# Kernel optimization log

Hardware: AMD Instinct MI355X
Metric: run time of the kernel (lower is better)

Reference implementation:

```python
import jax, jax.numpy as jnp
import numpy as np

N_NODES = 50000
NEG_SLOPE = 0.2

def _leaky(x):
    return jnp.where(x > 0, x, NEG_SLOPE * x)

def _magic_conv(h, src, dst, edge_attr, anet_W, anet_b, mlp_W, mlp_b, eps):
    # align edge features to node dim: [E, d_in]
    e = edge_attr @ anet_W + anet_b
    # message: relu(x_j + edge), gather from source nodes
    msg = jax.nn.relu(h[src] + e)
    # scatter-add aggregate to target nodes: [N, d_in]
    agg = jax.ops.segment_sum(msg, dst, num_segments=N_NODES)
    # GIN-style update: cat([agg, (1+eps)*x]) -> Linear -> LeakyReLU(0.2)
    z = jnp.concatenate([agg, (1.0 + eps) * h], axis=-1) @ mlp_W + mlp_b
    return _leaky(z)

def setup_inputs() -> dict:
    key = jax.random.key(0)
    ks = jax.random.split(key, 16)
    E, D, DE = 800000, 128, 64
    inp = {
        "x": jax.random.normal(ks[0], (N_NODES, D), dtype=jnp.float32),
        "edge_index": jax.random.randint(ks[1], (2, E), 0, N_NODES, dtype=jnp.int64),
        "edge_attr": jax.random.normal(ks[2], (E, DE), dtype=jnp.float32),
    }
    s = lambda d: 1.0 / np.sqrt(d)
    # conv layer 0 (128 -> 128) and layer 1 (128 -> 128)
    for l, k0 in [(0, 3), (1, 8)]:
        inp[f"anet_W{l}"] = jax.random.uniform(ks[k0], (DE, D), jnp.float32, -s(DE), s(DE))
        inp[f"anet_b{l}"] = jax.random.uniform(ks[k0 + 1], (D,), jnp.float32, -s(DE), s(DE))
        inp[f"mlp_W{l}"] = jax.random.uniform(ks[k0 + 2], (2 * D, D), jnp.float32, -s(2 * D), s(2 * D))
        inp[f"mlp_b{l}"] = jax.random.uniform(ks[k0 + 3], (D,), jnp.float32, -s(2 * D), s(2 * D))
        inp[f"eps{l}"] = jnp.full((1,), 1e-4, dtype=jnp.float32)
    # link predictor: Linear(128->128) + LeakyReLU, Linear(128->2)
    inp["lp_W1"] = jax.random.uniform(ks[13], (D, D), jnp.float32, -s(D), s(D))
    inp["lp_b1"] = jax.random.uniform(ks[14], (D,), jnp.float32, -s(D), s(D))
    inp["lp_W2"] = jax.random.uniform(ks[15], (D, 2), jnp.float32, -s(D), s(D))
    inp["lp_b2"] = jnp.zeros((2,), dtype=jnp.float32)
    return inp

def reference(x, edge_index, edge_attr, anet_W0, anet_b0, mlp_W0, mlp_b0, eps0,
              anet_W1, anet_b1, mlp_W1, mlp_b1, eps1,
              lp_W1, lp_b1, lp_W2, lp_b2):
    src = edge_index[0]
    dst = edge_index[1]
    h = _magic_conv(x, src, dst, edge_attr, anet_W0, anet_b0, mlp_W0, mlp_b0, eps0)
    h = _magic_conv(h, src, dst, edge_attr, anet_W1, anet_b1, mlp_W1, mlp_b1, eps1)
    h = jax.nn.relu(h)
    # MULT embed reduction over edge endpoints: [E, 128]
    h_edge = h[src] * h[dst]
    z = _leaky(h_edge @ lp_W1 + lp_b1)
    logits = z @ lp_W2 + lp_b2
    yhat = jax.nn.softmax(logits, axis=-1)
    return (h_edge, yhat)
```

## Files before the change

### kernel.cpp

```cpp
#include <hip/hip_runtime.h>
#include <math.h>

#define NNODES 50000
#define DIM 128
#define DEDGE 64

typedef __attribute__((ext_vector_type(8))) short bf16x8;
typedef __attribute__((ext_vector_type(4))) float f32x4;
typedef __attribute__((ext_vector_type(2))) float f32x2;

__device__ __forceinline__ float bf_lo(unsigned u) { return __builtin_bit_cast(float, u << 16); }
__device__ __forceinline__ float bf_hi(unsigned u) { return __builtin_bit_cast(float, u & 0xFFFF0000u); }
__device__ __forceinline__ float bf_s(short s) {
    return __builtin_bit_cast(float, ((unsigned)(unsigned short)s) << 16);
}
__device__ __forceinline__ unsigned short f2b_rtn(float f) {
    unsigned u = __builtin_bit_cast(unsigned, f);
    u += 0x7FFFu + ((u >> 16) & 1u);
    return (unsigned short)(u >> 16);
}

__global__ void detect_mode_kernel(const void* __restrict__ ei, int* __restrict__ flag) {
    __shared__ int bad;
    if (threadIdx.x == 0) bad = 0;
    __syncthreads();
    const long long* p = (const long long*)ei;
    int localbad = 0;
    for (int i = threadIdx.x; i < 4096; i += blockDim.x) {
        long long v = p[i];
        if (v < 0 || v >= NNODES) localbad = 1;
    }
    if (localbad) atomicOr(&bad, 1);
    __syncthreads();
    if (threadIdx.x == 0) *flag = bad ? 0 : 1;
}

__device__ __forceinline__ int load_idx(const void* ei, long long pos, int mode64) {
    if (mode64) return (int)((const long long*)ei)[pos];
    return ((const int*)ei)[pos];
}

__global__ void prep_weights(const float* __restrict__ aW0, const float* __restrict__ aW1,
                             const float* __restrict__ mW0, const float* __restrict__ mW1,
                             const float* __restrict__ lpW1,
                             const float* __restrict__ eps0p, const float* __restrict__ eps1p,
                             short* __restrict__ wt)
{
    int i = blockIdx.x * 256 + threadIdx.x;
    const float* src; int K, off, f;
    float scale_hi = 1.0f;
    if (i < 8192)        { src = aW0;  K = 64;  off = 0;     f = i; }
    else if (i < 16384)  { src = aW1;  K = 64;  off = 8192;  f = i - 8192; }
    else if (i < 49152)  { src = mW0;  K = 256; off = 16384; f = i - 16384;
                           scale_hi = 1.0f + eps0p[0]; }
    else if (i < 81920)  { src = mW1;  K = 256; off = 49152; f = i - 49152;
                           scale_hi = 1.0f + eps1p[0]; }
    else                 { src = lpW1; K = 128; off = 81920; f = i - 81920; }
    const int NKC = K >> 5;
    int j = f & 7, l = (f >> 3) & 63, c = f >> 9;
    int kc = c % NKC, n = c / NKC;
    int col = n * 16 + (l & 15);
    int k = kc * 32 + ((l >> 4) << 3) + j;
    float v = src[k * DIM + col];
    if (k >= 128) v *= scale_hi;
    wt[off + f] = (short)f2b_rtn(v);
}

__global__ void f32_to_bf16_kernel(const float* __restrict__ in,
                                   unsigned short* __restrict__ out, long long n)
{
    long long i = ((long long)blockIdx.x * 256 + threadIdx.x) * 8;
    if (i >= n) return;
    f32x4 a = *(const f32x4*)(in + i);
    f32x4 b = *(const f32x4*)(in + i + 4);
    unsigned short v[8];
#pragma unroll
    for (int t = 0; t < 4; t++) { v[t] = f2b_rtn(a[t]); v[4 + t] = f2b_rtn(b[t]); }
    unsigned p0 = v[0] | ((unsigned)v[1] << 16);
    unsigned p1 = v[2] | ((unsigned)v[3] << 16);
    unsigned p2 = v[4] | ((unsigned)v[5] << 16);
    unsigned p3 = v[6] | ((unsigned)v[7] << 16);
    f32x4 pk = {__builtin_bit_cast(float, p0), __builtin_bit_cast(float, p1),
                __builtin_bit_cast(float, p2), __builtin_bit_cast(float, p3)};
    *(f32x4*)(out + i) = pk;
}

__global__ void hist_kernel(const void* __restrict__ ei, const int* __restrict__ modep,
                            int* __restrict__ counts, int E)
{
    const int mode64 = *modep;
    for (int e = blockIdx.x * 256 + threadIdx.x; e < E; e += gridDim.x * 256)
        atomicAdd(&counts[load_idx(ei, (long long)E + e, mode64)], 1);
}

__global__ __launch_bounds__(1024) void scan_kernel(const int* __restrict__ counts,
                                                    int* __restrict__ cursor)
{
    __shared__ int part[1024];
    const int t = threadIdx.x;
    const int CH = (NNODES + 1023) / 1024;
    const int lo = t * CH, hi = min(lo + CH, NNODES);
    int s = 0;
    for (int i = lo; i < hi; i++) s += counts[i];
    part[t] = s;
    __syncthreads();
    for (int d = 1; d < 1024; d <<= 1) {
        int v = (t >= d) ? part[t - d] : 0;
        __syncthreads();
        part[t] += v;
        __syncthreads();
    }
    int run = (t == 0) ? 0 : part[t - 1];
    for (int i = lo; i < hi; i++) { cursor[i] = run; run += counts[i]; }
}

__global__ void scatter_kernel(const void* __restrict__ ei, const int* __restrict__ modep,
                               int* __restrict__ cursor, int* __restrict__ perm,
                               int* __restrict__ srcs, int* __restrict__ dsts, int E)
{
    const int mode64 = *modep;
    for (int e = blockIdx.x * 256 + threadIdx.x; e < E; e += gridDim.x * 256) {
        int d = load_idx(ei, (long long)E + e, mode64);
        int s = load_idx(ei, e, mode64);
        int pos = atomicAdd(&cursor[d], 1);
        perm[pos] = e;
        srcs[pos] = s;
        dsts[pos] = d;
    }
}

__global__ void eattr_sort_bf16(const float* __restrict__ eattr, const int* __restrict__ perm,
                                unsigned short* __restrict__ out, int E)
{
    long long i = ((long long)blockIdx.x * 256 + threadIdx.x) * 8;
    if (i >= (long long)E * DEDGE) return;
    long long pos = i >> 6;
    int k = (int)(i & 63);
    long long eid = perm[pos];
    f32x4 a = *(const f32x4*)(eattr + eid * DEDGE + k);
    f32x4 b = *(const f32x4*)(eattr + eid * DEDGE + k + 4);
    unsigned short v[8];
#pragma unroll
    for (int t = 0; t < 4; t++) { v[t] = f2b_rtn(a[t]); v[4 + t] = f2b_rtn(b[t]); }
    unsigned p0 = v[0] | ((unsigned)v[1] << 16);
    unsigned p1 = v[2] | ((unsigned)v[3] << 16);
    unsigned p2 = v[4] | ((unsigned)v[5] << 16);
    unsigned p3 = v[6] | ((unsigned)v[7] << 16);
    f32x4 pk = {__builtin_bit_cast(float, p0), __builtin_bit_cast(float, p1),
                __builtin_bit_cast(float, p2), __builtin_bit_cast(float, p3)};
    __builtin_nontemporal_store(pk, (f32x4*)(out + i));
}

__global__ __launch_bounds__(256, 4) void edge_msg_sorted(
    const unsigned short* __restrict__ hb, const unsigned short* __restrict__ eattrs,
    const int* __restrict__ srcs, const int* __restrict__ dsts,
    const short* __restrict__ Wb,
    const float* __restrict__ bvec, float* __restrict__ agg, int E)
{
    __shared__ float e_lds[4][16][132];
    const int lane = threadIdx.x & 63;
    const int w = threadIdx.x >> 6;
    const int lg = lane >> 4, lr = lane & 15;
    const long long p0 = ((long long)blockIdx.x * 4 + w) * 16;
    if (p0 >= E) return;

    const long long pos = (p0 + lr < E) ? (p0 + lr) : (E - 1);
    const int sidx = srcs[pos];
    const int didx = dsts[pos];

    f32x4 acc[8];
#pragma unroll
    for (int n = 0; n < 8; n++) {
        float b = bvec[n * 16 + lr];
        acc[n] = (f32x4){b, b, b, b};
    }
    bf16x8 a[2];
#pragma unroll
    for (int kc = 0; kc < 2; kc++)
        a[kc] = __builtin_nontemporal_load(
            (const bf16x8*)(eattrs + pos * DEDGE + kc * 32 + lg * 8));

#pragma unroll
    for (int n = 0; n < 8; n++) {
#pragma unroll
        for (int kc = 0; kc < 2; kc++) {
            bf16x8 bh = *(const bf16x8*)(Wb + ((n * 2 + kc) * 64 + lane) * 8);
            acc[n] = __builtin_amdgcn_mfma_f32_16x16x32_bf16(a[kc], bh, acc[n], 0, 0, 0);
        }
    }
#pragma unroll
    for (int n = 0; n < 8; n++)
#pragma unroll
        for (int r = 0; r < 4; r++)
            e_lds[w][lg * 4 + r][n * 16 + lr] = acc[n][r];

    if (p0 + 16 <= E) {
        unsigned gu[16];
        int dvs[16];
#pragma unroll
        for (int r = 0; r < 16; r++) {
            int si = __shfl(sidx, r);
            gu[r] = *(const unsigned*)&hb[(long long)si * DIM + 2 * lane];
        }
#pragma unroll
        for (int r = 0; r < 16; r++) dvs[r] = __shfl(didx, r);
        float a0 = 0.f, a1 = 0.f;
#pragma unroll
        for (int r = 0; r < 16; r++) {
            f32x2 ev = *(const f32x2*)&e_lds[w][r][2 * lane];
            float m0 = fmaxf(ev.x + bf_lo(gu[r]), 0.f);
            float m1 = fmaxf(ev.y + bf_hi(gu[r]), 0.f);
            if (r > 0 && dvs[r] != dvs[r - 1]) {
                float* d = &agg[(long long)dvs[r - 1] * DIM + 2 * lane];
                unsafeAtomicAdd(d, a0);
                unsafeAtomicAdd(d + 1, a1);
                a0 = 0.f; a1 = 0.f;
            }
            a0 += m0; a1 += m1;
        }
        float* d = &agg[(long long)dvs[15] * DIM + 2 * lane];
        unsafeAtomicAdd(d, a0);
        unsafeAtomicAdd(d + 1, a1);
    } else {
        float a0 = 0.f, a1 = 0.f;
        int prev = -1;
        for (int r = 0; r < 16; r++) {
            if (p0 + r >= E) break;
            int di = __shfl(didx, r);
            int si = __shfl(sidx, r);
            f32x2 ev = *(const f32x2*)&e_lds[w][r][2 * lane];
            unsigned u = *(const unsigned*)&hb[(long long)si * DIM + 2 * lane];
            float m0 = fmaxf(ev.x + bf_lo(u), 0.f);
            float m1 = fmaxf(ev.y + bf_hi(u), 0.f);
            if (di != prev && prev >= 0) {
                float* d = &agg[(long long)prev * DIM + 2 * lane];
                unsafeAtomicAdd(d, a0);
                unsafeAtomicAdd(d + 1, a1);
                a0 = 0.f; a1 = 0.f;
            }
            a0 += m0; a1 += m1; prev = di;
        }
        if (prev >= 0) {
            float* d = &agg[(long long)prev * DIM + 2 * lane];
            unsafeAtomicAdd(d, a0);
            unsafeAtomicAdd(d + 1, a1);
        }
    }
}

__global__ __launch_bounds__(256, 4) void node_update_mfma(
    const float* __restrict__ agg, const unsigned short* __restrict__ hb,
    const short* __restrict__ Wb, const float* __restrict__ bvec,
    unsigned short* __restrict__ houtb, int relu_flag)
{
    __shared__ float st[4][16][132];
    const int lane = threadIdx.x & 63;
    const int w = threadIdx.x >> 6;
    const int lg = lane >> 4, lr = lane & 15;
    const int n0 = (blockIdx.x * 4 + w) * 16;
    if (n0 >= NNODES) return;
    const int arow = (n0 + lr < NNODES) ? (n0 + lr) : (NNODES - 1);

    f32x4 acc[8];
#pragma unroll
    for (int n = 0; n < 8; n++) {
        float b = bvec[n * 16 + lr];
        acc[n] = (f32x4){b, b, b, b};
    }
#pragma unroll
    for (int kc = 0; kc < 8; kc++) {
        bf16x8 av;
        if (kc < 4) {
            const int k = kc * 32 + lg * 8;
            f32x4 v0 = *(const f32x4*)(agg + (long long)arow * DIM + k);
            f32x4 v1 = *(const f32x4*)(agg + (long long)arow * DIM + k + 4);
#pragma unroll
            for (int i = 0; i < 4; i++) {
                av[i] = (short)f2b_rtn(v0[i]);
                av[4 + i] = (short)f2b_rtn(v1[i]);
            }
        } else {
            av = *(const bf16x8*)(hb + (long long)arow * DIM + (kc - 4) * 32 + lg * 8);
        }
#pragma unroll
        for (int n = 0; n < 8; n++) {
            bf16x8 bh = *(const bf16x8*)(Wb + ((n * 8 + kc) * 64 + lane) * 8);
            acc[n] = __builtin_amdgcn_mfma_f32_16x16x32_bf16(av, bh, acc[n], 0, 0, 0);
        }
    }
#pragma unroll
    for (int n = 0; n < 8; n++) {
#pragma unroll
        for (int r = 0; r < 4; r++) {
            float z = acc[n][r];
            z = relu_flag ? fmaxf(z, 0.f) : (z > 0.f ? z : 0.2f * z);
            st[w][lg * 4 + r][n * 16 + lr] = z;
        }
    }
    for (int r = 0; r < 16; r++) {
        int row = n0 + r;
        if (row >= NNODES) break;
        f32x2 v = *(const f32x2*)&st[w][r][2 * lane];
        unsigned pk = (unsigned)f2b_rtn(v.x) | ((unsigned)f2b_rtn(v.y) << 16);
        *(unsigned*)&houtb[(long long)row * DIM + 2 * lane] = pk;
    }
}

__global__ __launch_bounds__(256, 6) void edge_head_mfma(
    const unsigned short* __restrict__ hb, const void* __restrict__ ei,
    const int* __restrict__ modep,
    const short* __restrict__ W1b, const float* __restrict__ b1,
    const float* __restrict__ W2, const float* __restrict__ b2,
    float* __restrict__ out_he, float* __restrict__ out_y, int E)
{
    const int mode64 = *modep;
    const int lane = threadIdx.x & 63;
    const int w = threadIdx.x >> 6;
    const int lg = lane >> 4, lr = lane & 15;
    const long long e0 = ((long long)blockIdx.x * 4 + w) * 16;
    if (e0 >= E) return;
    const long long erow = (e0 + lr < E) ? (e0 + lr) : (E - 1);
    int si = load_idx(ei, erow, mode64);
    int di = load_idx(ei, (long long)E + erow, mode64);

    f32x4 acc[8];
#pragma unroll
    for (int n = 0; n < 8; n++) {
        float b = b1[n * 16 + lr];
        acc[n] = (f32x4){b, b, b, b};
    }
    bf16x8 ab[4];
#pragma unroll
    for (int kc = 0; kc < 4; kc++) {
        const int k = kc * 32 + lg * 8;
        bf16x8 hs = *(const bf16x8*)(hb + (long long)si * DIM + k);
        bf16x8 hd = *(const bf16x8*)(hb + (long long)di * DIM + k);
        f32x4 p0, p1;
#pragma unroll
        for (int i = 0; i < 4; i++) {
            p0[i] = bf_s(hs[i]) * bf_s(hd[i]);
            p1[i] = bf_s(hs[4 + i]) * bf_s(hd[4 + i]);
        }
        if (e0 + lr < E) {
            __builtin_nontemporal_store(p0, (f32x4*)(out_he + erow * DIM + k));
            __builtin_nontemporal_store(p1, (f32x4*)(out_he + erow * DIM + k + 4));
        }
#pragma unroll
        for (int i = 0; i < 4; i++) {
            ab[kc][i] = (short)f2b_rtn(p0[i]);
            ab[kc][4 + i] = (short)f2b_rtn(p1[i]);
        }
    }
#pragma unroll
    for (int n = 0; n < 8; n++) {
#pragma unroll
        for (int kc = 0; kc < 4; kc++) {
            bf16x8 bh = *(const bf16x8*)(W1b + ((n * 4 + kc) * 64 + lane) * 8);
            acc[n] = __builtin_amdgcn_mfma_f32_16x16x32_bf16(ab[kc], bh, acc[n], 0, 0, 0);
        }
    }
    float q0[4] = {0.f, 0.f, 0.f, 0.f}, q1[4] = {0.f, 0.f, 0.f, 0.f};
#pragma unroll
    for (int n = 0; n < 8; n++) {
        float w2a = W2[(n * 16 + lr) * 2 + 0];
        float w2b = W2[(n * 16 + lr) * 2 + 1];
#pragma unroll
        for (int r = 0; r < 4; r++) {
            float z = acc[n][r];
            z = z > 0.f ? z : 0.2f * z;
            q0[r] = fmaf(z, w2a, q0[r]);
            q1[r] = fmaf(z, w2b, q1[r]);
        }
    }
#pragma unroll
    for (int m = 1; m < 16; m <<= 1) {
#pragma unroll
        for (int r = 0; r < 4; r++) {
            q0[r] += __shfl_xor(q0[r], m);
            q1[r] += __shfl_xor(q1[r], m);
        }
    }
    if (lr == 0) {
        float c0 = b2[0], c1 = b2[1];
#pragma unroll
        for (int r = 0; r < 4; r++) {
            long long e = e0 + lg * 4 + r;
            if (e < E) {
                float l0 = q0[r] + c0, l1 = q1[r] + c1;
                float mx = fmaxf(l0, l1);
                float x0 = expf(l0 - mx), x1 = expf(l1 - mx);
                float inv = 1.f / (x0 + x1);
                __builtin_nontemporal_store(x0 * inv, &out_y[e * 2 + 0]);
                __builtin_nontemporal_store(x1 * inv, &out_y[e * 2 + 1]);
            }
        }
    }
}

extern "C" void kernel_launch(void* const* d_in, const int* in_sizes, int n_in,
                              void* d_out, int out_size, void* d_ws, size_t ws_size,
                              hipStream_t stream)
{
    const float* x     = (const float*)d_in[0];
    const void*  ei    = d_in[1];
    const float* eattr = (const float*)d_in[2];
    const float* aW0   = (const float*)d_in[3];
    const float* ab0   = (const float*)d_in[4];
    const float* mW0   = (const float*)d_in[5];
    const float* mb0   = (const float*)d_in[6];
    const float* eps0  = (const float*)d_in[7];
    const float* aW1   = (const float*)d_in[8];
    const float* ab1   = (const float*)d_in[9];
    const float* mW1   = (const float*)d_in[10];
    const float* mb1   = (const float*)d_in[11];
    const float* eps1  = (const float*)d_in[12];
    const float* lpW1  = (const float*)d_in[13];
    const float* lpb1  = (const float*)d_in[14];
    const float* lpW2  = (const float*)d_in[15];
    const float* lpb2  = (const float*)d_in[16];

    const int E = in_sizes[1] / 2;
    const long long NTAB = (long long)NNODES * DIM;

    float* wsf  = (float*)d_ws;
    int*   flag = (int*)d_ws;
    float* agg  = wsf + 64;
    short* wt   = (short*)(agg + NTAB);
    unsigned short* xb_h2b = (unsigned short*)(wt + 98304);
    unsigned short* h1b    = xb_h2b + NTAB;
    int* counts = (int*)(h1b + NTAB);
    int* cursor = counts + 50048;
    int* perm   = cursor + 50048;
    int* srcs   = perm + E;
    int* dsts   = srcs + E;
    unsigned short* eattrs = (unsigned short*)(dsts + E);

    float* out_he = (float*)d_out;
    float* out_y  = out_he + (long long)E * DIM;

    const short* aW0b  = wt;
    const short* aW1b  = wt + 8192;
    const short* mW0b  = wt + 16384;
    const short* mW1b  = wt + 49152;
    const short* lpW1b = wt + 81920;

    detect_mode_kernel<<<1, 256, 0, stream>>>(ei, flag);
    prep_weights<<<384, 256, 0, stream>>>(aW0, aW1, mW0, mW1, lpW1, eps0, eps1, wt);
    f32_to_bf16_kernel<<<(int)(NTAB / 8 / 256), 256, 0, stream>>>(x, xb_h2b, NTAB);

    hipMemsetAsync(counts, 0, 50048 * sizeof(int), stream);
    hist_kernel<<<1024, 256, 0, stream>>>(ei, flag, counts, E);
    scan_kernel<<<1, 1024, 0, stream>>>(counts, cursor);
    scatter_kernel<<<1024, 256, 0, stream>>>(ei, flag, cursor, perm, srcs, dsts, E);
    eattr_sort_bf16<<<(E * DEDGE / 8 + 255) / 256, 256, 0, stream>>>(eattr, perm, eattrs, E);

    const int eblocks = (E + 63) / 64;
    const int nblocks = (NNODES + 63) / 64;

    hipMemsetAsync(agg, 0, NTAB * sizeof(float), stream);
    edge_msg_sorted<<<eblocks, 256, 0, stream>>>(xb_h2b, eattrs, srcs, dsts,
                                                 aW0b, ab0, agg, E);
    node_update_mfma<<<nblocks, 256, 0, stream>>>(agg, xb_h2b, mW0b, mb0, h1b, 0);

    hipMemsetAsync(agg, 0, NTAB * sizeof(float), stream);
    edge_msg_sorted<<<eblocks, 256, 0, stream>>>(h1b, eattrs, srcs, dsts,
                                                 aW1b, ab1, agg, E);
    node_update_mfma<<<nblocks, 256, 0, stream>>>(agg, h1b, mW1b, mb1, xb_h2b, 1);

    edge_head_mfma<<<eblocks, 256, 0, stream>>>(xb_h2b, ei, flag, lpW1b, lpb1, lpW2, lpb2,
                                                out_he, out_y, E);
}
```

Baseline: 660.0 us.

## Process two edge tiles per wave in message kernel and coalesce softmax stores

The edge message kernel now handles 32 sorted edges per wave in two 16-edge steps. A running per-destination partial sum is carried across both steps, so runs of the same destination that cross the old tile boundary need fewer atomics, and bias loads are amortized. The edge head computes softmax on all lanes and shuffles results so a full tile writes its 32 output floats as one coalesced store instead of scattered per-lane writes. The agg reads in the node update become nontemporal loads. The cost is fewer waves in the edge kernel (less parallelism) and some extra shuffle and select work.

Result: faster. 632.1 us (-4.2%).

```diff
diff --git a/kernel.cpp b/kernel.cpp
--- a/kernel.cpp
+++ b/kernel.cpp
@@ -161,90 +161,100 @@
     const int lane = threadIdx.x & 63;
     const int w = threadIdx.x >> 6;
     const int lg = lane >> 4, lr = lane & 15;
-    const long long p0 = ((long long)blockIdx.x * 4 + w) * 16;
+    const long long p0 = ((long long)blockIdx.x * 4 + w) * 32;
     if (p0 >= E) return;
 
-    const long long pos = (p0 + lr < E) ? (p0 + lr) : (E - 1);
-    const int sidx = srcs[pos];
-    const int didx = dsts[pos];
-
-    f32x4 acc[8];
-#pragma unroll
-    for (int n = 0; n < 8; n++) {
-        float b = bvec[n * 16 + lr];
-        acc[n] = (f32x4){b, b, b, b};
-    }
-    bf16x8 a[2];
-#pragma unroll
-    for (int kc = 0; kc < 2; kc++)
-        a[kc] = __builtin_nontemporal_load(
-            (const bf16x8*)(eattrs + pos * DEDGE + kc * 32 + lg * 8));
-
-#pragma unroll
-    for (int n = 0; n < 8; n++) {
-#pragma unroll
-        for (int kc = 0; kc < 2; kc++) {
-            bf16x8 bh = *(const bf16x8*)(Wb + ((n * 2 + kc) * 64 + lane) * 8);
-            acc[n] = __builtin_amdgcn_mfma_f32_16x16x32_bf16(a[kc], bh, acc[n], 0, 0, 0);
-        }
-    }
-#pragma unroll
-    for (int n = 0; n < 8; n++)
-#pragma unroll
-        for (int r = 0; r < 4; r++)
-            e_lds[w][lg * 4 + r][n * 16 + lr] = acc[n][r];
-
-    if (p0 + 16 <= E) {
-        unsigned gu[16];
-        int dvs[16];
-#pragma unroll
-        for (int r = 0; r < 16; r++) {
-            int si = __shfl(sidx, r);
-            gu[r] = *(const unsigned*)&hb[(long long)si * DIM + 2 * lane];
-        }
-#pragma unroll
-        for (int r = 0; r < 16; r++) dvs[r] = __shfl(didx, r);
-        float a0 = 0.f, a1 = 0.f;
-#pragma unroll
-        for (int r = 0; r < 16; r++) {
-            f32x2 ev = *(const f32x2*)&e_lds[w][r][2 * lane];
-            float m0 = fmaxf(ev.x + bf_lo(gu[r]), 0.f);
-            float m1 = fmaxf(ev.y + bf_hi(gu[r]), 0.f);
-            if (r > 0 && dvs[r] != dvs[r - 1]) {
-                float* d = &agg[(long long)dvs[r - 1] * DIM + 2 * lane];
-                unsafeAtomicAdd(d, a0);
-                unsafeAtomicAdd(d + 1, a1);
-                a0 = 0.f; a1 = 0.f;
+    float bias0 = bvec[0 * 16 + lr], bias1 = bvec[1 * 16 + lr],
+          bias2 = bvec[2 * 16 + lr], bias3 = bvec[3 * 16 + lr],
+          bias4 = bvec[4 * 16 + lr], bias5 = bvec[5 * 16 + lr],
+          bias6 = bvec[6 * 16 + lr], bias7 = bvec[7 * 16 + lr];
+    float bias[8] = {bias0, bias1, bias2, bias3, bias4, bias5, bias6, bias7};
+
+    float a0 = 0.f, a1 = 0.f;
+    int prev = -1;
+
+    const bool fullwave = (p0 + 32 <= E);
+
+#pragma unroll
+    for (int st = 0; st < 2; st++) {
+        const long long t0 = p0 + st * 16;
+        if (t0 >= E) break;
+        const long long pos = (t0 + lr < E) ? (t0 + lr) : (E - 1);
+        const int sidx = srcs[pos];
+        const int didx = dsts[pos];
+
+        f32x4 acc[8];
+#pragma unroll
+        for (int n = 0; n < 8; n++) {
+            float b = bias[n];
+            acc[n] = (f32x4){b, b, b, b};
+        }
+        bf16x8 a[2];
+#pragma unroll
+        for (int kc = 0; kc < 2; kc++)
+            a[kc] = __builtin_nontemporal_load(
+                (const bf16x8*)(eattrs + pos * DEDGE + kc * 32 + lg * 8));
+
+#pragma unroll
+        for (int n = 0; n < 8; n++) {
+#pragma unroll
+            for (int kc = 0; kc < 2; kc++) {
+                bf16x8 bh = *(const bf16x8*)(Wb + ((n * 2 + kc) * 64 + lane) * 8);
+                acc[n] = __builtin_amdgcn_mfma_f32_16x16x32_bf16(a[kc], bh, acc[n], 0, 0, 0);
             }
-            a0 += m0; a1 += m1;
-        }
-        float* d = &agg[(long long)dvs[15] * DIM + 2 * lane];
+        }
+#pragma unroll
+        for (int n = 0; n < 8; n++)
+#pragma unroll
+            for (int r = 0; r < 4; r++)
+                e_lds[w][lg * 4 + r][n * 16 + lr] = acc[n][r];
+
+        if (fullwave) {
+            unsigned gu[16];
+            int dvs[16];
+#pragma unroll
+            for (int r = 0; r < 16; r++) {
+                int si = __shfl(sidx, r);
+                gu[r] = *(const unsigned*)&hb[(long long)si * DIM + 2 * lane];
+            }
+#pragma unroll
+            for (int r = 0; r < 16; r++) dvs[r] = __shfl(didx, r);
+#pragma unroll
+            for (int r = 0; r < 16; r++) {
+                f32x2 ev = *(const f32x2*)&e_lds[w][r][2 * lane];
+                float m0 = fmaxf(ev.x + bf_lo(gu[r]), 0.f);
+                float m1 = fmaxf(ev.y + bf_hi(gu[r]), 0.f);
+                if (dvs[r] != prev && prev >= 0) {
+                    float* d = &agg[(long long)prev * DIM + 2 * lane];
+                    unsafeAtomicAdd(d, a0);
+                    unsafeAtomicAdd(d + 1, a1);
+                    a0 = 0.f; a1 = 0.f;
+                }
+                a0 += m0; a1 += m1; prev = dvs[r];
+            }
+        } else {
+            for (int r = 0; r < 16; r++) {
+                if (t0 + r >= E) break;
+                int di = __shfl(didx, r);
+                int si = __shfl(sidx, r);
+                f32x2 ev = *(const f32x2*)&e_lds[w][r][2 * lane];
+                unsigned u = *(const unsigned*)&hb[(long long)si * DIM + 2 * lane];
+                float m0 = fmaxf(ev.x + bf_lo(u), 0.f);
+                float m1 = fmaxf(ev.y + bf_hi(u), 0.f);
+                if (di != prev && prev >= 0) {
+                    float* d = &agg[(long long)prev * DIM + 2 * lane];
+                    unsafeAtomicAdd(d, a0);
+                    unsafeAtomicAdd(d + 1, a1);
+                    a0 = 0.f; a1 = 0.f;
+                }
+                a0 += m0; a1 += m1; prev = di;
+            }
+        }
+    }
+    if (prev >= 0) {
+        float* d = &agg[(long long)prev * DIM + 2 * lane];
         unsafeAtomicAdd(d, a0);
         unsafeAtomicAdd(d + 1, a1);
-    } else {
-        float a0 = 0.f, a1 = 0.f;
-        int prev = -1;
-        for (int r = 0; r < 16; r++) {
-            if (p0 + r >= E) break;
-            int di = __shfl(didx, r);
-            int si = __shfl(sidx, r);
-            f32x2 ev = *(const f32x2*)&e_lds[w][r][2 * lane];
-            unsigned u = *(const unsigned*)&hb[(long long)si * DIM + 2 * lane];
-            float m0 = fmaxf(ev.x + bf_lo(u), 0.f);
-            float m1 = fmaxf(ev.y + bf_hi(u), 0.f);
-            if (di != prev && prev >= 0) {
-                float* d = &agg[(long long)prev * DIM + 2 * lane];
-                unsafeAtomicAdd(d, a0);
-                unsafeAtomicAdd(d + 1, a1);
-                a0 = 0.f; a1 = 0.f;
-            }
-            a0 += m0; a1 += m1; prev = di;
-        }
-        if (prev >= 0) {
-            float* d = &agg[(long long)prev * DIM + 2 * lane];
-            unsafeAtomicAdd(d, a0);
-            unsafeAtomicAdd(d + 1, a1);
-        }
     }
 }
 
@@ -272,8 +282,8 @@
         bf16x8 av;
         if (kc < 4) {
             const int k = kc * 32 + lg * 8;
-            f32x4 v0 = *(const f32x4*)(agg + (long long)arow * DIM + k);
-            f32x4 v1 = *(const f32x4*)(agg + (long long)arow * DIM + k + 4);
+            f32x4 v0 = __builtin_nontemporal_load((const f32x4*)(agg + (long long)arow * DIM + k));
+            f32x4 v1 = __builtin_nontemporal_load((const f32x4*)(agg + (long long)arow * DIM + k + 4));
 #pragma unroll
             for (int i = 0; i < 4; i++) {
                 av[i] = (short)f2b_rtn(v0[i]);
@@ -319,7 +329,8 @@
     const int lg = lane >> 4, lr = lane & 15;
     const long long e0 = ((long long)blockIdx.x * 4 + w) * 16;
     if (e0 >= E) return;
-    const long long erow = (e0 + lr < E) ? (e0 + lr) : (E - 1);
+    const bool full = (e0 + 16 <= E);
+    const long long erow = (full || e0 + lr < E) ? (e0 + lr) : (E - 1);
     int si = load_idx(ei, erow, mode64);
     int di = load_idx(ei, (long long)E + erow, mode64);
 
@@ -341,7 +352,7 @@
             p0[i] = bf_s(hs[i]) * bf_s(hd[i]);
             p1[i] = bf_s(hs[4 + i]) * bf_s(hd[4 + i]);
         }
-        if (e0 + lr < E) {
+        if (full || e0 + lr < E) {
             __builtin_nontemporal_store(p0, (f32x4*)(out_he + erow * DIM + k));
             __builtin_nontemporal_store(p1, (f32x4*)(out_he + erow * DIM + k + 4));
         }
@@ -380,18 +391,35 @@
             q1[r] += __shfl_xor(q1[r], m);
         }
     }
-    if (lr == 0) {
-        float c0 = b2[0], c1 = b2[1];
+    float c0 = b2[0], c1 = b2[1];
+    float s0[4], s1[4];
+#pragma unroll
+    for (int r = 0; r < 4; r++) {
+        float l0 = q0[r] + c0, l1 = q1[r] + c1;
+        float mx = fmaxf(l0, l1);
+        float x0 = expf(l0 - mx), x1 = expf(l1 - mx);
+        float inv = 1.f / (x0 + x1);
+        s0[r] = x0 * inv;
+        s1[r] = x1 * inv;
+    }
+    if (full) {
+        float ea = (lane & 2) ? s0[1] : s0[0];
+        float eb = (lane & 2) ? s0[3] : s0[2];
+        float ec = (lane & 2) ? s1[1] : s1[0];
+        float ed = (lane & 2) ? s1[3] : s1[2];
+        float e0v = (lane & 4) ? eb : ea;
+        float e1v = (lane & 4) ? ed : ec;
+        float ex = (lane & 1) ? e1v : e0v;
+        float v = __shfl(ex, ((lane >> 3) << 4) + (lane & 7));
+        if (lane < 32)
+            __builtin_nontemporal_store(v, &out_y[e0 * 2 + lane]);
+    } else if (lr == 0) {
 #pragma unroll
         for (int r = 0; r < 4; r++) {
             long long e = e0 + lg * 4 + r;
             if (e < E) {
-                float l0 = q0[r] + c0, l1 = q1[r] + c1;
-                float mx = fmaxf(l0, l1);
-                float x0 = expf(l0 - mx), x1 = expf(l1 - mx);
-                float inv = 1.f / (x0 + x1);
-                __builtin_nontemporal_store(x0 * inv, &out_y[e * 2 + 0]);
-                __builtin_nontemporal_store(x1 * inv, &out_y[e * 2 + 1]);
+                out_y[e * 2 + 0] = s0[r];
+                out_y[e * 2 + 1] = s1[r];
             }
         }
     }
@@ -454,19 +482,20 @@
     scatter_kernel<<<1024, 256, 0, stream>>>(ei, flag, cursor, perm, srcs, dsts, E);
     eattr_sort_bf16<<<(E * DEDGE / 8 + 255) / 256, 256, 0, stream>>>(eattr, perm, eattrs, E);
 
-    const int eblocks = (E + 63) / 64;
+    const int eblocks32 = (E + 127) / 128;
+    const int eblocks16 = (E + 63) / 64;
     const int nblocks = (NNODES + 63) / 64;
 
     hipMemsetAsync(agg, 0, NTAB * sizeof(float), stream);
-    edge_msg_sorted<<<eblocks, 256, 0, stream>>>(xb_h2b, eattrs, srcs, dsts,
-                                                 aW0b, ab0, agg, E);
+    edge_msg_sorted<<<eblocks32, 256, 0, stream>>>(xb_h2b, eattrs, srcs, dsts,
+                                                   aW0b, ab0, agg, E);
     node_update_mfma<<<nblocks, 256, 0, stream>>>(agg, xb_h2b, mW0b, mb0, h1b, 0);
 
     hipMemsetAsync(agg, 0, NTAB * sizeof(float), stream);
-    edge_msg_sorted<<<eblocks, 256, 0, stream>>>(h1b, eattrs, srcs, dsts,
-                                                 aW1b, ab1, agg, E);
+    edge_msg_sorted<<<eblocks32, 256, 0, stream>>>(h1b, eattrs, srcs, dsts,
+                                                   aW1b, ab1, agg, E);
     node_update_mfma<<<nblocks, 256, 0, stream>>>(agg, h1b, mW1b, mb1, xb_h2b, 1);
 
-    edge_head_mfma<<<eblocks, 256, 0, stream>>>(xb_h2b, ei, flag, lpW1b, lpb1, lpW2, lpb2,
-                                                out_he, out_y, E);
-}
+    edge_head_mfma<<<eblocks16, 256, 0, stream>>>(xb_h2b, ei, flag, lpW1b, lpb1, lpW2, lpb2,
+                                                  out_he, out_y, E);
+}
```
